# Kernel tuning notes

Hardware: AMD Instinct MI355X
Metric: run time of the kernel (lower is better)

The kernel has to match this reference:

```python
import jax, jax.numpy as jnp
import numpy as np

N = 100000   # nodes
F = 256      # input features
H = 64       # hidden dims
C = 40       # classes
L = 4        # GGNN layers
E = 1200000  # edges


def setup_inputs() -> dict:
    key = jax.random.key(0)
    ks = jax.random.split(key, 8)
    x = jax.random.normal(ks[0], (N, F), dtype=jnp.float32)
    edge_index = jax.random.randint(ks[1], (2, E), 0, N, dtype=jnp.int64)
    # glorot-initialized projection weights
    weight_in = jax.random.uniform(ks[2], (F, H), jnp.float32, -1.0, 1.0) * np.sqrt(6.0 / (F + H))
    weight_out = jax.random.uniform(ks[3], (H, C), jnp.float32, -1.0, 1.0) * np.sqrt(6.0 / (H + C))
    # GatedGraphConv: per-layer message weight [L, H, H], shared GRUCell params
    conv_weight = jax.random.uniform(ks[4], (L, H, H), jnp.float32, -1.0, 1.0) * np.sqrt(6.0 / (2 * H))
    s = 1.0 / np.sqrt(H)
    w_ih = jax.random.uniform(ks[5], (3 * H, H), jnp.float32, -s, s)
    w_hh = jax.random.uniform(ks[6], (3 * H, H), jnp.float32, -s, s)
    b_ih = jax.random.uniform(ks[7], (3 * H,), jnp.float32, -s, s)
    b_hh = jnp.zeros((3 * H,), jnp.float32)
    return {"x": x, "edge_index": edge_index, "weight_in": weight_in,
            "weight_out": weight_out, "conv_weight": conv_weight,
            "w_ih": w_ih, "w_hh": w_hh, "b_ih": b_ih, "b_hh": b_hh}


def _gru_cell(a, h, w_ih, w_hh, b_ih, b_hh):
    # torch.nn.GRUCell math: input a, hidden h
    gi = a @ w_ih.T + b_ih
    gh = h @ w_hh.T + b_hh
    i_r, i_z, i_n = jnp.split(gi, 3, axis=1)
    h_r, h_z, h_n = jnp.split(gh, 3, axis=1)
    r = jax.nn.sigmoid(i_r + h_r)
    z = jax.nn.sigmoid(i_z + h_z)
    n = jnp.tanh(i_n + r * h_n)
    return (1.0 - z) * n + z * h


def reference(x, edge_index, weight_in, weight_out, conv_weight, w_ih, w_hh, b_ih, b_hh):
    n_nodes = x.shape[0]
    src, dst = edge_index[0], edge_index[1]
    h = x @ weight_in  # [N, H]
    for i in range(conv_weight.shape[0]):
        m = h @ conv_weight[i]                                   # [N, H]
        agg = jax.ops.segment_sum(m[src], dst, num_segments=n_nodes)  # scatter-add
        h = _gru_cell(agg, h, w_ih, w_hh, b_ih, b_hh)
    out = h @ weight_out  # [N, C]
    return jax.nn.log_softmax(out, axis=1)
```

## Files before the change

kernel.cpp:

```cpp
#include <hip/hip_runtime.h>


#define DEVI __device__ __forceinline__

typedef __attribute__((ext_vector_type(8))) short short8;
typedef __attribute__((ext_vector_type(4))) float f32x4;

constexpr int N_NODES   = 100000;
constexpr int F_IN      = 256;
constexpr int H_DIM     = 64;
constexpr int C_OUT     = 40;
constexpr int ROW_TILES = N_NODES / 16;
constexpr int CH        = 8192;
constexpr int NBUCK     = (N_NODES + 127) / 128;
constexpr int LB_STRIDE = NBUCK + 1;
constexpr int BCAP      = 2048;

DEVI float bf2f(unsigned short u) {
    unsigned v = ((unsigned)u) << 16;
    float f; __builtin_memcpy(&f, &v, 4); return f;
}
DEVI unsigned short f2bf(float f) {
    unsigned u; __builtin_memcpy(&u, &f, 4);
    unsigned r = u + 0x7FFFu + ((u >> 16) & 1u);
    return (unsigned short)(r >> 16);
}
DEVI float in_elem(const void* p, size_t idx, int f32flag) {
    return f32flag ? ((const float*)p)[idx]
                   : bf2f(((const unsigned short*)p)[idx]);
}
DEVI short8 f32row_to_frag(const float* __restrict__ p) {
    const f32x4* q = (const f32x4*)p;
    f32x4 lo = q[0], hi = q[1];
    short8 a;
    a[0] = (short)f2bf(lo[0]); a[1] = (short)f2bf(lo[1]);
    a[2] = (short)f2bf(lo[2]); a[3] = (short)f2bf(lo[3]);
    a[4] = (short)f2bf(hi[0]); a[5] = (short)f2bf(hi[1]);
    a[6] = (short)f2bf(hi[2]); a[7] = (short)f2bf(hi[3]);
    return a;
}

__global__ void detect_kernel(const void* x, const int* ei, int* flags) {
    if (threadIdx.x != 0 || blockIdx.x != 0) return;
    const unsigned short* u = (const unsigned short*)x;
    int sane = 0;
    for (int i = 0; i < 256; ++i) {
        int e = (u[i] >> 7) & 0xFF;
        if (e >= 100 && e <= 145) sane++;
    }
    flags[0] = (sane < 230) ? 1 : 0;
    int zeros = 0;
    for (int i = 0; i < 64; ++i)
        if (ei[2 * i + 1] == 0) zeros++;
    flags[1] = (zeros >= 63) ? 1 : 0;
}

__global__ __launch_bounds__(256) void bucket_local(
        const int* __restrict__ ei, int E, const int* __restrict__ flags,
        int* __restrict__ wgsorted,
        int* __restrict__ lbase_g) {
    __shared__ int hist[NBUCK];
    __shared__ int partial[256];
    __shared__ int staging[CH];
    int tid = threadIdx.x, wg = blockIdx.x;
    int i64 = flags[1];
    int base = wg * CH;
    int cnt_wg = min(CH, E - base);

    for (int i = tid; i < NBUCK; i += 256) hist[i] = 0;
    __syncthreads();
    for (int k = tid; k < cnt_wg; k += 256) {
        size_t e = (size_t)base + k;
        int d = i64 ? ei[2 * ((size_t)E + e)] : ei[(size_t)E + e];
        atomicAdd(&hist[d >> 7], 1);
    }
    __syncthreads();
    int i0 = 4 * tid;
    int e0 = (i0 + 0 < NBUCK) ? hist[i0 + 0] : 0;
    int e1 = (i0 + 1 < NBUCK) ? hist[i0 + 1] : 0;
    int e2 = (i0 + 2 < NBUCK) ? hist[i0 + 2] : 0;
    int e3 = (i0 + 3 < NBUCK) ? hist[i0 + 3] : 0;
    int s0 = e0, s1 = s0 + e1, s2 = s1 + e2, s3 = s2 + e3;
    __syncthreads();
    partial[tid] = s3;
    __syncthreads();
    for (int ofs = 1; ofs < 256; ofs <<= 1) {
        int add = (tid >= ofs) ? partial[tid - ofs] : 0;
        __syncthreads();
        partial[tid] += add;
        __syncthreads();
    }
    int pbase = (tid > 0) ? partial[tid - 1] : 0;
    if (i0 + 0 < NBUCK) hist[i0 + 0] = pbase;
    if (i0 + 1 < NBUCK) hist[i0 + 1] = pbase + s0;
    if (i0 + 2 < NBUCK) hist[i0 + 2] = pbase + s1;
    if (i0 + 3 < NBUCK) hist[i0 + 3] = pbase + s2;
    __syncthreads();
    int* lb = lbase_g + (size_t)wg * LB_STRIDE;
    for (int i = tid; i < NBUCK; i += 256) lb[i] = hist[i];
    if (tid == 0) lb[NBUCK] = cnt_wg;
    __syncthreads();
    for (int k = tid; k < cnt_wg; k += 256) {
        size_t e = (size_t)base + k;
        int s, d;
        if (i64) { s = ei[2 * e]; d = ei[2 * ((size_t)E + e)]; }
        else     { s = ei[e];     d = ei[(size_t)E + e]; }
        int pos = atomicAdd(&hist[d >> 7], 1);
        staging[pos] = ((d & 127) << 17) | s;
    }
    __syncthreads();
    for (int k = tid; k < cnt_wg; k += 256)
        wgsorted[(size_t)base + k] = staging[k];
}

__global__ __launch_bounds__(256) void bucket_csr(
        const int* __restrict__ wgsorted,
        const int* __restrict__ lbase_g,
        int nwg,
        int* __restrict__ rowptr,
        int* __restrict__ counts,
        int* __restrict__ esrc) {
    __shared__ int segofs[256];
    __shared__ int edata[BCAP];
    __shared__ int sout[BCAP];
    __shared__ int hist2[128];
    __shared__ int cur2[128];
    int tid = threadIdx.x, b = blockIdx.x;

    int lbv = 0, cntv = 0;
    if (tid < nwg) {
        const int* lb = lbase_g + (size_t)tid * LB_STRIDE;
        lbv  = lb[b];
        cntv = lb[b + 1] - lbv;
    }
    segofs[tid] = cntv;
    __syncthreads();
    for (int ofs = 1; ofs < 256; ofs <<= 1) {
        int add = (tid >= ofs) ? segofs[tid - ofs] : 0;
        __syncthreads();
        segofs[tid] += add;
        __syncthreads();
    }
    int tot = segofs[255];
    int myofs = (tid > 0) ? segofs[tid - 1] : 0;
    if (tot > BCAP) tot = BCAP;
    if (tid < nwg && cntv > 0) {
        const int* srcp = wgsorted + (size_t)tid * CH + lbv;
        for (int i = 0; i < cntv; ++i) {
            int o = myofs + i;
            if (o < BCAP) edata[o] = srcp[i];
        }
    }
    if (tid < 128) hist2[tid] = 0;
    __syncthreads();
    for (int i = tid; i < tot; i += 256) atomicAdd(&hist2[edata[i] >> 17], 1);
    __syncthreads();
    if (tid < 128) cur2[tid] = hist2[tid];
    __syncthreads();
    for (int ofs = 1; ofs < 128; ofs <<= 1) {
        int add = 0;
        if (tid < 128 && tid >= ofs) add = cur2[tid - ofs];
        __syncthreads();
        if (tid < 128) cur2[tid] += add;
        __syncthreads();
    }
    int nodeexcl = 0;
    if (tid < 128) nodeexcl = (tid > 0) ? cur2[tid - 1] : 0;
    __syncthreads();
    if (tid < 128) {
        int node = b * 128 + tid;
        if (node < N_NODES) {
            counts[node] = hist2[tid];
            rowptr[node] = b * BCAP + nodeexcl;
        }
        cur2[tid] = nodeexcl;
    }
    __syncthreads();
    for (int i = tid; i < tot; i += 256) {
        int p = edata[i];
        int pos = atomicAdd(&cur2[p >> 17], 1);
        sout[pos] = p & 0x1FFFF;
    }
    __syncthreads();
    for (int i = tid; i < tot; i += 256)
        esrc[(size_t)b * BCAP + i] = sout[i];
}

__global__ void prep_bfrag(const void* __restrict__ src,
                           unsigned short* __restrict__ dst,
                           int K, int npad_tiles, int ncols_real,
                           const int* __restrict__ flags) {
    int f32 = flags[0];
    int t = blockIdx.x * blockDim.x + threadIdx.x;
    int total = (K / 32) * npad_tiles * 512;
    if (t >= total) return;
    int i    = t & 7;
    int lane = (t >> 3) & 63;
    int jt   = (t >> 9) % npad_tiles;
    int kb   = t / (512 * npad_tiles);
    int k    = kb * 32 + ((lane >> 4) << 3) + i;
    int col  = jt * 16 + (lane & 15);
    unsigned short v = 0;
    if (col < ncols_real) v = f2bf(in_elem(src, (size_t)k * ncols_real + col, f32));
    dst[t] = v;
}

__global__ __launch_bounds__(64) void wcomb_kernel(
        const void* __restrict__ conv_w, const void* __restrict__ w_ih,
        unsigned short* __restrict__ wcomb, const int* __restrict__ flags) {
    int f32 = flags[0];
    int lane = threadIdx.x;
    int c = blockIdx.x;
    int l = blockIdx.y;
    int kb = c / 12, jt = c % 12;
    int quad = lane >> 4, l15 = lane & 15;
    int g = jt * 16 + l15;
    unsigned short* dst = wcomb + (size_t)l * 12288 + ((size_t)c * 64 + lane) * 8;
#pragma unroll
    for (int i = 0; i < 8; ++i) {
        int k = kb * 32 + quad * 8 + i;
        float acc = 0.0f;
        for (int j = 0; j < 64; ++j)
            acc += in_elem(conv_w, (size_t)l * 4096 + k * 64 + j, f32) *
                   in_elem(w_ih, (size_t)g * 64 + j, f32);
        dst[i] = f2bf(acc);
    }
}

__global__ void prep_gruw(const void* __restrict__ w_hh,
                          const void* __restrict__ b_ih,
                          const void* __restrict__ b_hh,
                          unsigned short* __restrict__ whh_c,
                          unsigned short* __restrict__ bias_c,
                          const int* __restrict__ flags) {
    int f32 = flags[0];
    int t = blockIdx.x * blockDim.x + threadIdx.x;
    if (t < 12288)            whh_c[t]          = f2bf(in_elem(w_hh, t, f32));
    else if (t < 12288 + 192) bias_c[t - 12288] = f2bf(in_elem(b_ih, t - 12288, f32));
    else if (t < 12288 + 384) bias_c[t - 12288] = f2bf(in_elem(b_hh, t - 12480, f32));
}

template <int XF32>
DEVI void proj_in_body(const void* __restrict__ xr,
                       const unsigned short* __restrict__ wfrag,
                       unsigned short* __restrict__ h) {
    int wid = blockIdx.x * 4 + (threadIdx.x >> 6);
    if (wid >= ROW_TILES) return;
    int lane = threadIdx.x & 63;
    int l15 = lane & 15, quad = lane >> 4;
    int row0 = wid * 16;
    int arow = row0 + l15;

    f32x4 acc[4];
#pragma unroll
    for (int jt = 0; jt < 4; ++jt) acc[jt] = (f32x4)(0.0f);

#pragma unroll
    for (int kb = 0; kb < 8; ++kb) {
        short8 a;
        if (XF32)
            a = f32row_to_frag((const float*)xr + (size_t)arow * F_IN + kb * 32 + quad * 8);
        else
            a = *(const short8*)((const unsigned short*)xr + (size_t)arow * F_IN + kb * 32 + quad * 8);
#pragma unroll
        for (int jt = 0; jt < 4; ++jt) {
            short8 b = *(const short8*)(wfrag + (size_t)((kb * 4 + jt) * 64 + lane) * 8);
            acc[jt] = __builtin_amdgcn_mfma_f32_16x16x32_bf16(a, b, acc[jt], 0, 0, 0);
        }
    }
#pragma unroll
    for (int jt = 0; jt < 4; ++jt)
#pragma unroll
        for (int r = 0; r < 4; ++r)
            h[(size_t)(row0 + quad * 4 + r) * H_DIM + jt * 16 + l15] = f2bf(acc[jt][r]);
}

__global__ __launch_bounds__(256) void proj_in_kernel(
        const void* __restrict__ x,
        const unsigned short* __restrict__ wfrag,
        unsigned short* __restrict__ h,
        const int* __restrict__ flags) {
    if (flags[0]) proj_in_body<1>(x, wfrag, h);
    else          proj_in_body<0>(x, wfrag, h);
}

__global__ __launch_bounds__(256) void gather_agg(
        const unsigned short* __restrict__ h,
        const int* __restrict__ rowptr,
        const int* __restrict__ counts,
        const int* __restrict__ esrc,
        unsigned short* __restrict__ aggB) {
    int n = blockIdx.x * 4 + (threadIdx.x >> 6);
    if (n >= N_NODES) return;
    int j = threadIdx.x & 63;
    int start = rowptr[n];
    int deg   = counts[n];
    float a0 = 0.f, a1 = 0.f, a2 = 0.f, a3 = 0.f;
    int i = 0;
    for (; i + 4 <= deg; i += 4) {
        int s0 = esrc[start + i],     s1 = esrc[start + i + 1];
        int s2 = esrc[start + i + 2], s3 = esrc[start + i + 3];
        a0 += bf2f(h[(size_t)s0 * H_DIM + j]);
        a1 += bf2f(h[(size_t)s1 * H_DIM + j]);
        a2 += bf2f(h[(size_t)s2 * H_DIM + j]);
        a3 += bf2f(h[(size_t)s3 * H_DIM + j]);
    }
    for (; i < deg; ++i)
        a0 += bf2f(h[(size_t)esrc[start + i] * H_DIM + j]);
    aggB[(size_t)n * H_DIM + j] = f2bf((a0 + a1) + (a2 + a3));
}

__global__ __launch_bounds__(256) void gru_kernel(
        const unsigned short* __restrict__ aggB,
        unsigned short* __restrict__ h,
        const unsigned short* __restrict__ wcomb_l,
        const unsigned short* __restrict__ whh_c,
        const unsigned short* __restrict__ bias_c) {
    int wid = blockIdx.x * 4 + (threadIdx.x >> 6);
    if (wid >= ROW_TILES) return;
    int lane = threadIdx.x & 63;
    int l15 = lane & 15, quad = lane >> 4;
    int row0 = wid * 16;
    int arow = row0 + l15;

    f32x4 gi[12], gh[12];
#pragma unroll
    for (int jt = 0; jt < 12; ++jt) { gi[jt] = (f32x4)(0.0f); gh[jt] = (f32x4)(0.0f); }

#pragma unroll
    for (int kb = 0; kb < 2; ++kb) {
        short8 aa = *(const short8*)(aggB + (size_t)arow * H_DIM + kb * 32 + quad * 8);
        short8 ah = *(const short8*)(h + (size_t)arow * H_DIM + kb * 32 + quad * 8);
#pragma unroll
        for (int jt = 0; jt < 12; ++jt) {
            short8 bi = *(const short8*)(wcomb_l + (size_t)((kb * 12 + jt) * 64 + lane) * 8);
            gi[jt] = __builtin_amdgcn_mfma_f32_16x16x32_bf16(aa, bi, gi[jt], 0, 0, 0);
            short8 bh = *(const short8*)(whh_c + (size_t)(jt * 16 + l15) * H_DIM + kb * 32 + quad * 8);
            gh[jt] = __builtin_amdgcn_mfma_f32_16x16x32_bf16(ah, bh, gh[jt], 0, 0, 0);
        }
    }

#pragma unroll
    for (int jc = 0; jc < 4; ++jc) {
        int j = jc * 16 + l15;
        float bir = bf2f(bias_c[j]),       bhr = bf2f(bias_c[192 + j]);
        float biz = bf2f(bias_c[64 + j]),  bhz = bf2f(bias_c[256 + j]);
        float bin = bf2f(bias_c[128 + j]), bhn = bf2f(bias_c[320 + j]);
#pragma unroll
        for (int r = 0; r < 4; ++r) {
            int row = row0 + quad * 4 + r;
            float xr = (gi[jc][r] + bir) + (gh[jc][r] + bhr);
            float xz = (gi[4 + jc][r] + biz) + (gh[4 + jc][r] + bhz);
            float in_ = gi[8 + jc][r] + bin;
            float hn_ = gh[8 + jc][r] + bhn;
            xr = fminf(fmaxf(xr, -30.0f), 30.0f);
            xz = fminf(fmaxf(xz, -30.0f), 30.0f);
            float rg = 1.0f / (1.0f + __expf(-xr));
            float zg = 1.0f / (1.0f + __expf(-xz));
            float na = in_ + rg * hn_;
            float ey = __expf(-2.0f * fabsf(na));
            float th = (1.0f - ey) / (1.0f + ey);
            float nt = (na < 0.0f) ? -th : th;
            float ho = bf2f(h[(size_t)row * H_DIM + j]);
            h[(size_t)row * H_DIM + j] = f2bf((1.0f - zg) * nt + zg * ho);
        }
    }
}

__global__ __launch_bounds__(256) void projout_kernel(
        const unsigned short* __restrict__ h,
        const unsigned short* __restrict__ wofrag,
        void* __restrict__ out,
        const int* __restrict__ flags) {
    int f32out = flags[0];
    int wid = blockIdx.x * 4 + (threadIdx.x >> 6);
    if (wid >= ROW_TILES) return;
    int lane = threadIdx.x & 63;
    int l15 = lane & 15, quad = lane >> 4;
    int row0 = wid * 16;
    int arow = row0 + l15;

    f32x4 acc[3];
#pragma unroll
    for (int jt = 0; jt < 3; ++jt) acc[jt] = (f32x4)(0.0f);

#pragma unroll
    for (int kb = 0; kb < 2; ++kb) {
        short8 a = *(const short8*)(h + (size_t)arow * H_DIM + kb * 32 + quad * 8);
#pragma unroll
        for (int jt = 0; jt < 3; ++jt) {
            short8 b = *(const short8*)(wofrag + (size_t)((kb * 3 + jt) * 64 + lane) * 8);
            acc[jt] = __builtin_amdgcn_mfma_f32_16x16x32_bf16(a, b, acc[jt], 0, 0, 0);
        }
    }

    float* of = (float*)out;
    unsigned short* ob = (unsigned short*)out;
    bool valid2 = (l15 < 8);
#pragma unroll
    for (int r = 0; r < 4; ++r) {
        int row = row0 + quad * 4 + r;
        float v0 = acc[0][r], v1 = acc[1][r], v2 = acc[2][r];
        float mx = fmaxf(v0, v1);
        if (valid2) mx = fmaxf(mx, v2);
#pragma unroll
        for (int d = 1; d < 16; d <<= 1) mx = fmaxf(mx, __shfl_xor(mx, d));
        float s = __expf(v0 - mx) + __expf(v1 - mx) + (valid2 ? __expf(v2 - mx) : 0.0f);
#pragma unroll
        for (int d = 1; d < 16; d <<= 1) s += __shfl_xor(s, d);
        float lg = mx + __logf(s);
        size_t o0 = (size_t)row * C_OUT + l15;
        if (f32out) {
            of[o0]      = v0 - lg;
            of[o0 + 16] = v1 - lg;
            if (valid2) of[o0 + 32] = v2 - lg;
        } else {
            ob[o0]      = f2bf(v0 - lg);
            ob[o0 + 16] = f2bf(v1 - lg);
            if (valid2) ob[o0 + 32] = f2bf(v2 - lg);
        }
    }
}

extern "C" void kernel_launch(void* const* d_in, const int* in_sizes, int n_in,
                              void* d_out, int out_size, void* d_ws, size_t ws_size,
                              hipStream_t stream) {
    const void* x      = d_in[0];
    const int*  ei     = (const int*)d_in[1];
    const void* w_in   = d_in[2];
    const void* w_out  = d_in[3];
    const void* conv_w = d_in[4];
    const void* w_ih   = d_in[5];
    const void* w_hh   = d_in[6];
    const void* b_ih   = d_in[7];
    const void* b_hh   = d_in[8];

    const int E   = in_sizes[1] / 2;
    const int nwg = (E + CH - 1) / CH;

    char* ws = (char*)d_ws;
    size_t off = 0;
    auto carve = [&](size_t bytes) {
        void* p = ws + off;
        off += (bytes + 255) & ~(size_t)255;
        return p;
    };
    int*            flags    = (int*)carve(256);
    unsigned short* aggB     = (unsigned short*)carve((size_t)N_NODES * H_DIM * 2);
    unsigned short* hbuf     = (unsigned short*)carve((size_t)N_NODES * H_DIM * 2);
    int*            counts   = (int*)carve((size_t)N_NODES * 4);
    int*            rowptr   = (int*)carve((size_t)N_NODES * 4);
    int*            wgsorted = (int*)carve((size_t)nwg * CH * 4);
    int*            lbase_g  = (int*)carve((size_t)nwg * LB_STRIDE * 4);
    int*            esrcP    = (int*)carve((size_t)NBUCK * BCAP * 4);
    unsigned short* winfrag  = (unsigned short*)carve((size_t)8 * 4 * 512 * 2);
    unsigned short* wcomb    = (unsigned short*)carve((size_t)4 * 12288 * 2);
    unsigned short* wofrag   = (unsigned short*)carve((size_t)3072 * 2);
    unsigned short* whh_c    = (unsigned short*)carve((size_t)12288 * 2);
    unsigned short* bias_c   = (unsigned short*)carve((size_t)384 * 2);

    detect_kernel<<<1, 64, 0, stream>>>(x, ei, flags);

    bucket_local<<<nwg, 256, 0, stream>>>(ei, E, flags, wgsorted, lbase_g);
    bucket_csr<<<NBUCK, 256, 0, stream>>>(wgsorted, lbase_g, nwg,
                                          rowptr, counts, esrcP);

    prep_bfrag<<<64, 256, 0, stream>>>(w_in, winfrag, 256, 4, 64, flags);
    prep_bfrag<<<12, 256, 0, stream>>>(w_out, wofrag, 64, 3, 40, flags);
    wcomb_kernel<<<dim3(24, 4), 64, 0, stream>>>(conv_w, w_ih, wcomb, flags);
    prep_gruw<<<50, 256, 0, stream>>>(w_hh, b_ih, b_hh, whh_c, bias_c, flags);

    const int gblocks = (ROW_TILES + 3) / 4;
    const int nblocks = N_NODES / 4;

    proj_in_kernel<<<gblocks, 256, 0, stream>>>(x, winfrag, hbuf, flags);

    for (int l = 0; l < 4; ++l) {
        gather_agg<<<nblocks, 256, 0, stream>>>(hbuf, rowptr, counts, esrcP, aggB);
        gru_kernel<<<gblocks, 256, 0, stream>>>(aggB, hbuf, wcomb + (size_t)l * 12288,
                                                whh_c, bias_c);
    }

    projout_kernel<<<gblocks, 256, 0, stream>>>(hbuf, wofrag, d_out, flags);
}
```

Baseline: 638.4 us.

## Fuse neighbor gather into GRU kernel with ping-pong hidden buffers

Merges the per-layer gather_agg and gru_kernel into one kernel. Each wave gathers neighbor rows for its 16-node tile with 8-byte vector loads, keeps the fp32 sums in shared memory, and feeds them straight into the MFMA GRU, so the aggB round trip through global memory and one launch per layer go away. The hidden state is double-buffered, so reads of the old h cannot race with writes. The CSR bucket copy now uses a parallel binary search over segments instead of a per-thread serial loop, and the small weight prep kernels are merged into one launch. The risk is load imbalance: each lane loops to the maximum degree across four nodes, which lowers gather parallelism compared with one wave per node.

After: 1.012 ms. 58.5% more time.

```diff
diff --git a/kernel.cpp b/kernel.cpp
--- a/kernel.cpp
+++ b/kernel.cpp
@@ -120,7 +120,8 @@
         int* __restrict__ rowptr,
         int* __restrict__ counts,
         int* __restrict__ esrc) {
-    __shared__ int segofs[256];
+    __shared__ int segincl[256];
+    __shared__ int segbase[256];
     __shared__ int edata[BCAP];
     __shared__ int sout[BCAP];
     __shared__ int hist2[128];
@@ -133,23 +134,24 @@
         lbv  = lb[b];
         cntv = lb[b + 1] - lbv;
     }
-    segofs[tid] = cntv;
+    segbase[tid] = lbv;
+    segincl[tid] = cntv;
     __syncthreads();
     for (int ofs = 1; ofs < 256; ofs <<= 1) {
-        int add = (tid >= ofs) ? segofs[tid - ofs] : 0;
+        int add = (tid >= ofs) ? segincl[tid - ofs] : 0;
         __syncthreads();
-        segofs[tid] += add;
+        segincl[tid] += add;
         __syncthreads();
     }
-    int tot = segofs[255];
-    int myofs = (tid > 0) ? segofs[tid - 1] : 0;
-    if (tot > BCAP) tot = BCAP;
-    if (tid < nwg && cntv > 0) {
-        const int* srcp = wgsorted + (size_t)tid * CH + lbv;
-        for (int i = 0; i < cntv; ++i) {
-            int o = myofs + i;
-            if (o < BCAP) edata[o] = srcp[i];
-        }
+    int tot = min(segincl[255], BCAP);
+    for (int i = tid; i < tot; i += 256) {
+        int lo = 0, hi = 255;
+        while (lo < hi) {
+            int mid = (lo + hi) >> 1;
+            if (segincl[mid] > i) hi = mid; else lo = mid + 1;
+        }
+        int excl = (lo > 0) ? segincl[lo - 1] : 0;
+        edata[i] = wgsorted[(size_t)lo * CH + segbase[lo] + (i - excl)];
     }
     if (tid < 128) hist2[tid] = 0;
     __syncthreads();
@@ -186,23 +188,41 @@
         esrc[(size_t)b * BCAP + i] = sout[i];
 }
 
-__global__ void prep_bfrag(const void* __restrict__ src,
-                           unsigned short* __restrict__ dst,
-                           int K, int npad_tiles, int ncols_real,
-                           const int* __restrict__ flags) {
+__global__ void prep_misc(const void* __restrict__ w_in,
+                          const void* __restrict__ w_out,
+                          const void* __restrict__ w_hh,
+                          const void* __restrict__ b_ih,
+                          const void* __restrict__ b_hh,
+                          unsigned short* __restrict__ winfrag,
+                          unsigned short* __restrict__ wofrag,
+                          unsigned short* __restrict__ whh_c,
+                          unsigned short* __restrict__ bias_c,
+                          const int* __restrict__ flags) {
     int f32 = flags[0];
     int t = blockIdx.x * blockDim.x + threadIdx.x;
-    int total = (K / 32) * npad_tiles * 512;
-    if (t >= total) return;
-    int i    = t & 7;
-    int lane = (t >> 3) & 63;
-    int jt   = (t >> 9) % npad_tiles;
-    int kb   = t / (512 * npad_tiles);
-    int k    = kb * 32 + ((lane >> 4) << 3) + i;
-    int col  = jt * 16 + (lane & 15);
-    unsigned short v = 0;
-    if (col < ncols_real) v = f2bf(in_elem(src, (size_t)k * ncols_real + col, f32));
-    dst[t] = v;
+    if (t < 16384) {
+        int i = t & 7, lane = (t >> 3) & 63, jt = (t >> 9) & 3, kb = t >> 11;
+        int k = kb * 32 + ((lane >> 4) << 3) + i;
+        int col = jt * 16 + (lane & 15);
+        winfrag[t] = f2bf(in_elem(w_in, (size_t)k * 64 + col, f32));
+    } else if (t < 16384 + 3072) {
+        int u = t - 16384;
+        int i = u & 7, lane = (u >> 3) & 63;
+        int jt = (u >> 9) % 3, kb = u / 1536;
+        int k = kb * 32 + ((lane >> 4) << 3) + i;
+        int col = jt * 16 + (lane & 15);
+        wofrag[u] = (col < 40) ? f2bf(in_elem(w_out, (size_t)k * 40 + col, f32))
+                               : (unsigned short)0;
+    } else if (t < 16384 + 3072 + 12288) {
+        int u = t - 16384 - 3072;
+        whh_c[u] = f2bf(in_elem(w_hh, u, f32));
+    } else if (t < 16384 + 3072 + 12288 + 192) {
+        int u = t - 16384 - 3072 - 12288;
+        bias_c[u] = f2bf(in_elem(b_ih, u, f32));
+    } else if (t < 16384 + 3072 + 12288 + 384) {
+        int u = t - 16384 - 3072 - 12288 - 192;
+        bias_c[192 + u] = f2bf(in_elem(b_hh, u, f32));
+    }
 }
 
 __global__ __launch_bounds__(64) void wcomb_kernel(
@@ -227,19 +247,6 @@
     }
 }
 
-__global__ void prep_gruw(const void* __restrict__ w_hh,
-                          const void* __restrict__ b_ih,
-                          const void* __restrict__ b_hh,
-                          unsigned short* __restrict__ whh_c,
-                          unsigned short* __restrict__ bias_c,
-                          const int* __restrict__ flags) {
-    int f32 = flags[0];
-    int t = blockIdx.x * blockDim.x + threadIdx.x;
-    if (t < 12288)            whh_c[t]          = f2bf(in_elem(w_hh, t, f32));
-    else if (t < 12288 + 192) bias_c[t - 12288] = f2bf(in_elem(b_ih, t - 12288, f32));
-    else if (t < 12288 + 384) bias_c[t - 12288] = f2bf(in_elem(b_hh, t - 12480, f32));
-}
-
 template <int XF32>
 DEVI void proj_in_body(const void* __restrict__ xr,
                        const unsigned short* __restrict__ wfrag,
@@ -284,44 +291,53 @@
     else          proj_in_body<0>(x, wfrag, h);
 }
 
-__global__ __launch_bounds__(256) void gather_agg(
-        const unsigned short* __restrict__ h,
+__global__ __launch_bounds__(256) void gru_fused(
+        const unsigned short* __restrict__ hin,
+        unsigned short* __restrict__ hout,
         const int* __restrict__ rowptr,
         const int* __restrict__ counts,
         const int* __restrict__ esrc,
-        unsigned short* __restrict__ aggB) {
-    int n = blockIdx.x * 4 + (threadIdx.x >> 6);
-    if (n >= N_NODES) return;
-    int j = threadIdx.x & 63;
-    int start = rowptr[n];
-    int deg   = counts[n];
-    float a0 = 0.f, a1 = 0.f, a2 = 0.f, a3 = 0.f;
-    int i = 0;
-    for (; i + 4 <= deg; i += 4) {
-        int s0 = esrc[start + i],     s1 = esrc[start + i + 1];
-        int s2 = esrc[start + i + 2], s3 = esrc[start + i + 3];
-        a0 += bf2f(h[(size_t)s0 * H_DIM + j]);
-        a1 += bf2f(h[(size_t)s1 * H_DIM + j]);
-        a2 += bf2f(h[(size_t)s2 * H_DIM + j]);
-        a3 += bf2f(h[(size_t)s3 * H_DIM + j]);
-    }
-    for (; i < deg; ++i)
-        a0 += bf2f(h[(size_t)esrc[start + i] * H_DIM + j]);
-    aggB[(size_t)n * H_DIM + j] = f2bf((a0 + a1) + (a2 + a3));
-}
-
-__global__ __launch_bounds__(256) void gru_kernel(
-        const unsigned short* __restrict__ aggB,
-        unsigned short* __restrict__ h,
         const unsigned short* __restrict__ wcomb_l,
         const unsigned short* __restrict__ whh_c,
         const unsigned short* __restrict__ bias_c) {
-    int wid = blockIdx.x * 4 + (threadIdx.x >> 6);
-    if (wid >= ROW_TILES) return;
+    __shared__ float aggT[4][16][68];
+    int warp = threadIdx.x >> 6;
     int lane = threadIdx.x & 63;
+    int wid = blockIdx.x * 4 + warp;
+    bool active = (wid < ROW_TILES);
+    int wids = active ? wid : (ROW_TILES - 1);
     int l15 = lane & 15, quad = lane >> 4;
-    int row0 = wid * 16;
-    int arow = row0 + l15;
+    int row0 = wids * 16;
+
+    int st[4], dg[4];
+    int mxd = 0;
+#pragma unroll
+    for (int it = 0; it < 4; ++it) {
+        int n = row0 + it * 4 + quad;
+        st[it] = rowptr[n];
+        dg[it] = active ? counts[n] : 0;
+        mxd = max(mxd, dg[it]);
+    }
+    f32x4 ac[4];
+#pragma unroll
+    for (int it = 0; it < 4; ++it) ac[it] = (f32x4)(0.0f);
+    for (int i = 0; i < mxd; ++i) {
+#pragma unroll
+        for (int it = 0; it < 4; ++it) {
+            if (i < dg[it]) {
+                int s = esrc[st[it] + i];
+                ushort4 u = *(const ushort4*)(hin + (size_t)s * H_DIM + l15 * 4);
+                ac[it][0] += bf2f(u.x);
+                ac[it][1] += bf2f(u.y);
+                ac[it][2] += bf2f(u.z);
+                ac[it][3] += bf2f(u.w);
+            }
+        }
+    }
+#pragma unroll
+    for (int it = 0; it < 4; ++it)
+        *(f32x4*)&aggT[warp][it * 4 + quad][l15 * 4] = ac[it];
+    __syncthreads();
 
     f32x4 gi[12], gh[12];
 #pragma unroll
@@ -329,8 +345,11 @@
 
 #pragma unroll
     for (int kb = 0; kb < 2; ++kb) {
-        short8 aa = *(const short8*)(aggB + (size_t)arow * H_DIM + kb * 32 + quad * 8);
-        short8 ah = *(const short8*)(h + (size_t)arow * H_DIM + kb * 32 + quad * 8);
+        short8 aa;
+#pragma unroll
+        for (int i = 0; i < 8; ++i)
+            aa[i] = (short)f2bf(aggT[warp][l15][kb * 32 + quad * 8 + i]);
+        short8 ah = *(const short8*)(hin + (size_t)(row0 + l15) * H_DIM + kb * 32 + quad * 8);
 #pragma unroll
         for (int jt = 0; jt < 12; ++jt) {
             short8 bi = *(const short8*)(wcomb_l + (size_t)((kb * 12 + jt) * 64 + lane) * 8);
@@ -361,8 +380,9 @@
             float ey = __expf(-2.0f * fabsf(na));
             float th = (1.0f - ey) / (1.0f + ey);
             float nt = (na < 0.0f) ? -th : th;
-            float ho = bf2f(h[(size_t)row * H_DIM + j]);
-            h[(size_t)row * H_DIM + j] = f2bf((1.0f - zg) * nt + zg * ho);
+            float ho = bf2f(hin[(size_t)row * H_DIM + j]);
+            if (active)
+                hout[(size_t)row * H_DIM + j] = f2bf((1.0f - zg) * nt + zg * ho);
         }
     }
 }
@@ -446,14 +466,14 @@
         return p;
     };
     int*            flags    = (int*)carve(256);
-    unsigned short* aggB     = (unsigned short*)carve((size_t)N_NODES * H_DIM * 2);
-    unsigned short* hbuf     = (unsigned short*)carve((size_t)N_NODES * H_DIM * 2);
+    unsigned short* h0       = (unsigned short*)carve((size_t)N_NODES * H_DIM * 2);
+    unsigned short* h1       = (unsigned short*)carve((size_t)N_NODES * H_DIM * 2);
     int*            counts   = (int*)carve((size_t)N_NODES * 4);
     int*            rowptr   = (int*)carve((size_t)N_NODES * 4);
     int*            wgsorted = (int*)carve((size_t)nwg * CH * 4);
     int*            lbase_g  = (int*)carve((size_t)nwg * LB_STRIDE * 4);
     int*            esrcP    = (int*)carve((size_t)NBUCK * BCAP * 4);
-    unsigned short* winfrag  = (unsigned short*)carve((size_t)8 * 4 * 512 * 2);
+    unsigned short* winfrag  = (unsigned short*)carve((size_t)16384 * 2);
     unsigned short* wcomb    = (unsigned short*)carve((size_t)4 * 12288 * 2);
     unsigned short* wofrag   = (unsigned short*)carve((size_t)3072 * 2);
     unsigned short* whh_c    = (unsigned short*)carve((size_t)12288 * 2);
@@ -465,21 +485,21 @@
     bucket_csr<<<NBUCK, 256, 0, stream>>>(wgsorted, lbase_g, nwg,
                                           rowptr, counts, esrcP);
 
-    prep_bfrag<<<64, 256, 0, stream>>>(w_in, winfrag, 256, 4, 64, flags);
-    prep_bfrag<<<12, 256, 0, stream>>>(w_out, wofrag, 64, 3, 40, flags);
+    prep_misc<<<(16384 + 3072 + 12288 + 384 + 255) / 256, 256, 0, stream>>>(
+        w_in, w_out, w_hh, b_ih, b_hh, winfrag, wofrag, whh_c, bias_c, flags);
     wcomb_kernel<<<dim3(24, 4), 64, 0, stream>>>(conv_w, w_ih, wcomb, flags);
-    prep_gruw<<<50, 256, 0, stream>>>(w_hh, b_ih, b_hh, whh_c, bias_c, flags);
 
     const int gblocks = (ROW_TILES + 3) / 4;
-    const int nblocks = N_NODES / 4;
-
-    proj_in_kernel<<<gblocks, 256, 0, stream>>>(x, winfrag, hbuf, flags);
-
+
+    proj_in_kernel<<<gblocks, 256, 0, stream>>>(x, winfrag, h0, flags);
+
+    unsigned short* hin = h0;
+    unsigned short* hout = h1;
     for (int l = 0; l < 4; ++l) {
-        gather_agg<<<nblocks, 256, 0, stream>>>(hbuf, rowptr, counts, esrcP, aggB);
-        gru_kernel<<<gblocks, 256, 0, stream>>>(aggB, hbuf, wcomb + (size_t)l * 12288,
-                                                whh_c, bias_c);
-    }
-
-    projout_kernel<<<gblocks, 256, 0, stream>>>(hbuf, wofrag, d_out, flags);
-}
+        gru_fused<<<gblocks, 256, 0, stream>>>(hin, hout, rowptr, counts, esrcP,
+                                               wcomb + (size_t)l * 12288, whh_c, bias_c);
+        unsigned short* t = hin; hin = hout; hout = t;
+    }
+
+    projout_kernel<<<gblocks, 256, 0, stream>>>(hin, wofrag, d_out, flags);
+}
```
